# Kernel tuning notes

Hardware: AMD Instinct MI355X
Metric: run time of the kernel (lower is better)

Reference implementation:

```python
import jax, jax.numpy as jnp
import numpy as np
from jax.ops import segment_sum

NEG_SLOPE = 0.01  # torch F.leaky_relu default

N_NODES = 100000
N_EDGES = 1600000
IN_FEAT = 67
HIDDEN = 256
N_CLASS = 18
N_GRAPHS = 256


def setup_inputs() -> dict:
    key = jax.random.key(0)
    ks = jax.random.split(key, 12)
    h = jax.random.normal(ks[0], (N_NODES, IN_FEAT), dtype=jnp.float32)
    src = jax.random.randint(ks[1], (N_EDGES,), 0, N_NODES, dtype=jnp.int32)
    dst = jax.random.randint(ks[2], (N_EDGES,), 0, N_NODES, dtype=jnp.int32)
    graph_ids = jnp.sort(jax.random.randint(ks[3], (N_NODES,), 0, N_GRAPHS, dtype=jnp.int32))
    s = 0.05
    W1_self = jax.random.normal(ks[4], (IN_FEAT, HIDDEN), dtype=jnp.float32) * s
    W1_neigh = jax.random.normal(ks[5], (IN_FEAT, HIDDEN), dtype=jnp.float32) * s
    b1 = jnp.zeros((HIDDEN,), dtype=jnp.float32)
    W2_self = jax.random.normal(ks[6], (HIDDEN, HIDDEN), dtype=jnp.float32) * s
    W2_neigh = jax.random.normal(ks[7], (HIDDEN, HIDDEN), dtype=jnp.float32) * s
    b2 = jnp.zeros((HIDDEN,), dtype=jnp.float32)
    Wfc = jax.random.normal(ks[8], (HIDDEN, N_CLASS), dtype=jnp.float32) * s
    bfc = jnp.zeros((N_CLASS,), dtype=jnp.float32)
    return {
        "h": h, "W1_self": W1_self, "W1_neigh": W1_neigh, "b1": b1,
        "W2_self": W2_self, "W2_neigh": W2_neigh, "b2": b2,
        "Wfc": Wfc, "bfc": bfc,
        "src": src, "dst": dst, "graph_ids": graph_ids, "num_graphs": N_GRAPHS,
    }


def _sage_mean(h, Wself, Wneigh, b, src, dst, n_nodes):
    # DGL SAGEConv(mean): h_neigh = mean over incoming neighbors; 0 if no neighbors
    agg = segment_sum(h[src], dst, num_segments=n_nodes)          # [N, D]
    deg = segment_sum(jnp.ones_like(dst, dtype=h.dtype), dst, num_segments=n_nodes)
    h_neigh = agg / jnp.maximum(deg, 1.0)[:, None]
    return h @ Wself + h_neigh @ Wneigh + b


def reference(h, W1_self, W1_neigh, b1, W2_self, W2_neigh, b2, Wfc, bfc,
              src, dst, graph_ids, num_graphs):
    n_nodes = h.shape[0]
    x = jax.nn.leaky_relu(_sage_mean(h, W1_self, W1_neigh, b1, src, dst, n_nodes), NEG_SLOPE)
    x = jax.nn.leaky_relu(_sage_mean(x, W2_self, W2_neigh, b2, src, dst, n_nodes), NEG_SLOPE)
    # dgl.mean_nodes: per-graph mean pooling over nodes
    gsum = segment_sum(x, graph_ids, num_segments=num_graphs)       # [G, D]
    gcnt = segment_sum(jnp.ones((n_nodes,), dtype=x.dtype), graph_ids, num_segments=num_graphs)
    hg = gsum / jnp.maximum(gcnt, 1.0)[:, None]
    return hg @ Wfc + bfc  # [G, n_classifier]
```

## Files before the change

kernel.cpp:

```cpp
#include <hip/hip_runtime.h>

#define WAVE 64
#define OW 256
#define LDA1 96
#define NCHUNK 64
#define PBITS 15
#define PBINS (1 << PBITS)
#define NPART 4

typedef short bf16x8 __attribute__((ext_vector_type(8)));
typedef float f32x4  __attribute__((ext_vector_type(4)));

__device__ __forceinline__ unsigned short f2bf(float f) {
    unsigned int u = __float_as_uint(f);
    u = (u + 0x7FFF + ((u >> 16) & 1)) >> 16;
    return (unsigned short)u;
}
__device__ __forceinline__ float bf2f(unsigned short u) {
    return __uint_as_float(((unsigned int)u) << 16);
}
__device__ __forceinline__ float bflo(unsigned int u) { return __uint_as_float(u << 16); }
__device__ __forceinline__ float bfhi(unsigned int u) { return __uint_as_float(u & 0xFFFF0000u); }
__device__ __forceinline__ unsigned int packbf(float lo, float hi) {
    return (unsigned int)f2bf(lo) | ((unsigned int)f2bf(hi) << 16);
}
__device__ __forceinline__ float lrelu(float x) { return x > 0.0f ? x : 0.01f * x; }


__device__ __forceinline__ void pack_b_body(const float* __restrict__ Ws,
                                            const float* __restrict__ Wn,
                                            unsigned short* __restrict__ Bb,
                                            int KHALF, int KT_HALF, int idx) {
    int e  = idx & 7;
    int l  = (idx >> 3) & 63;
    int nt = (idx >> 9) & 15;
    int kt = idx >> 13;
    int n  = nt * 16 + (l & 15);
    int kh = (kt < KT_HALF ? kt : kt - KT_HALF) * 32 + (l >> 4) * 8 + e;
    const float* W = (kt < KT_HALF) ? Ws : Wn;
    float v = (kh < KHALF) ? W[(size_t)kh * OW + n] : 0.0f;
    Bb[idx] = f2bf(v);
}

__global__ void prep_kernel(const float* __restrict__ h, unsigned int* __restrict__ hb,
                            int N, int K,
                            const float* __restrict__ W1s, const float* __restrict__ W1n,
                            unsigned short* __restrict__ Bb1,
                            const float* __restrict__ W2s, const float* __restrict__ W2n,
                            unsigned short* __restrict__ Bb2) {
    const int tid = blockIdx.x * blockDim.x + threadIdx.x;
    const int nth = gridDim.x * blockDim.x;

    const int tot_h = N * (LDA1 / 2);
    for (int i = tid; i < tot_h; i += nth) {
        int row = i / (LDA1 / 2);
        int c   = (i - row * (LDA1 / 2)) * 2;
        float v0 = (c     < K) ? h[(size_t)row * K + c]     : 0.0f;
        float v1 = (c + 1 < K) ? h[(size_t)row * K + c + 1] : 0.0f;
        hb[i] = packbf(v0, v1);
    }
    for (int i = tid; i < 2 * 3 * 16 * 64 * 8; i += nth)
        pack_b_body(W1s, W1n, Bb1, K, 3, i);
    for (int i = tid; i < 2 * 8 * 16 * 64 * 8; i += nth)
        pack_b_body(W2s, W2n, Bb2, OW, 8, i);
}


__global__ __launch_bounds__(512) void hist_kernel(const int* __restrict__ dst, int E, int N,
                                                   int* __restrict__ hist,
                                                   unsigned short* __restrict__ rank_local) {
    __shared__ unsigned int lcnt[PBINS / 2];
    const int c    = blockIdx.x / NPART;
    const int p    = blockIdx.x - c * NPART;
    const int base = p << PBITS;
    const int nb   = (N - base < PBINS) ? (N - base) : PBINS;
    if (nb <= 0) return;
    const int che = (E + NCHUNK - 1) / NCHUNK;
    const int beg = c * che;
    const int end = (beg + che < E) ? (beg + che) : E;

    for (int i = threadIdx.x; i < PBINS / 2; i += 512) lcnt[i] = 0;
    __syncthreads();

    for (int e = beg + (int)threadIdx.x; e < end; e += 512) {
        int d = dst[e] - base;
        if ((unsigned)d < (unsigned)nb) {
            unsigned int sh  = (d & 1) * 16;
            unsigned int old = atomicAdd(&lcnt[d >> 1], 1u << sh);
            rank_local[e] = (unsigned short)((old >> sh) & 0xFFFFu);
        }
    }
    __syncthreads();

    int* hrow = hist + (size_t)c * N + base;
    for (int i = threadIdx.x; i < nb; i += 512) {
        unsigned int v = lcnt[i >> 1];
        hrow[i] = (int)((v >> ((i & 1) * 16)) & 0xFFFFu);
    }
}

__global__ void chunk_scan_kernel(int* __restrict__ hist, int* __restrict__ cnt, int N) {
    int bin = blockIdx.x * blockDim.x + threadIdx.x;
    if (bin >= N) return;
    int s = 0;
#pragma unroll 8
    for (int c = 0; c < NCHUNK; ++c) {
        size_t idx = (size_t)c * N + bin;
        int t = hist[idx];
        hist[idx] = s;
        s += t;
    }
    cnt[bin] = s;
}

__global__ __launch_bounds__(1024) void scan_blocksum(const int* __restrict__ cnt,
                                                      int* __restrict__ bsum, int n) {
    __shared__ int s[1024];
    int i = blockIdx.x * 1024 + threadIdx.x;
    s[threadIdx.x] = (i < n) ? cnt[i] : 0;
    __syncthreads();
    for (int off = 512; off > 0; off >>= 1) {
        if (threadIdx.x < off) s[threadIdx.x] += s[threadIdx.x + off];
        __syncthreads();
    }
    if (threadIdx.x == 0) bsum[blockIdx.x] = s[0];
}

__global__ __launch_bounds__(128) void scan_offsets(int* __restrict__ bsum, int nb) {
    __shared__ int s[128];
    int v = (threadIdx.x < nb) ? bsum[threadIdx.x] : 0;
    s[threadIdx.x] = v;
    __syncthreads();
    for (int off = 1; off < 128; off <<= 1) {
        int t = (threadIdx.x >= off) ? s[threadIdx.x - off] : 0;
        __syncthreads();
        s[threadIdx.x] += t;
        __syncthreads();
    }
    if (threadIdx.x < nb) bsum[threadIdx.x] = s[threadIdx.x] - v;
}

__global__ __launch_bounds__(1024) void scan_write(const int* __restrict__ cnt,
                                                   const int* __restrict__ boff,
                                                   int* __restrict__ rowptr, int n) {
    __shared__ int s[1024];
    int i = blockIdx.x * 1024 + threadIdx.x;
    int v = (i < n) ? cnt[i] : 0;
    s[threadIdx.x] = v;
    __syncthreads();
    for (int off = 1; off < 1024; off <<= 1) {
        int t = (threadIdx.x >= off) ? s[threadIdx.x - off] : 0;
        __syncthreads();
        s[threadIdx.x] += t;
        __syncthreads();
    }
    if (i < n) rowptr[i + 1] = boff[blockIdx.x] + s[threadIdx.x];
    if (i == 0) rowptr[0] = 0;
}

__global__ void fill_kernel(const int* __restrict__ src, const int* __restrict__ dst,
                            const unsigned short* __restrict__ rank_local,
                            const int* __restrict__ rowptr, const int* __restrict__ hist,
                            int* __restrict__ csr, int E, int N) {
    const int che = (E + NCHUNK - 1) / NCHUNK;
    const int tid = blockIdx.x * blockDim.x + threadIdx.x;
    const int nth = gridDim.x * blockDim.x;
    for (int e = tid; e < E; e += nth) {
        int d = dst[e];
        int c = e / che;
        int pos = rowptr[d] + hist[(size_t)c * N + d] + (int)rank_local[e];
        csr[pos] = src[e];
    }
}


__global__ void gather_mean256_half(const unsigned int* __restrict__ feat,
                                    const int* __restrict__ rowptr, const int* __restrict__ csr,
                                    unsigned int* __restrict__ aggm, int N, int colhalf) {
    const int lane = threadIdx.x & (WAVE - 1);
    const int grp  = lane >> 4;
    const int sub  = lane & 15;
    const int cb   = colhalf * 64;
    int wave = (blockIdx.x * blockDim.x + threadIdx.x) / WAVE;
    int nw   = (gridDim.x * blockDim.x) / WAVE;

    for (int v = wave; v < N; v += nw) {
        const int beg = rowptr[v], deg = rowptr[v + 1] - beg;
        float l0 = 0.f, h0 = 0.f, l1 = 0.f, h1 = 0.f,
              l2 = 0.f, h2 = 0.f, l3 = 0.f, h3 = 0.f;

        const int noct = deg >> 3;
        for (int i = 0; i < noct; ++i) {
            int e0 = csr[beg + 8 * i + grp];
            int e1 = csr[beg + 8 * i + 4 + grp];
            uint4 x0 = *(const uint4*)(feat + (size_t)e0 * 128 + cb + sub * 4);
            uint4 x1 = *(const uint4*)(feat + (size_t)e1 * 128 + cb + sub * 4);
            l0 += bflo(x0.x) + bflo(x1.x); h0 += bfhi(x0.x) + bfhi(x1.x);
            l1 += bflo(x0.y) + bflo(x1.y); h1 += bfhi(x0.y) + bfhi(x1.y);
            l2 += bflo(x0.z) + bflo(x1.z); h2 += bfhi(x0.z) + bfhi(x1.z);
            l3 += bflo(x0.w) + bflo(x1.w); h3 += bfhi(x0.w) + bfhi(x1.w);
        }
        for (int e = (noct << 3) + grp; e < deg; e += 4) {
            int s = csr[beg + e];
            uint4 x = *(const uint4*)(feat + (size_t)s * 128 + cb + sub * 4);
            l0 += bflo(x.x); h0 += bfhi(x.x);
            l1 += bflo(x.y); h1 += bfhi(x.y);
            l2 += bflo(x.z); h2 += bfhi(x.z);
            l3 += bflo(x.w); h3 += bfhi(x.w);
        }
        l0 += __shfl_xor(l0, 16); l0 += __shfl_xor(l0, 32);
        h0 += __shfl_xor(h0, 16); h0 += __shfl_xor(h0, 32);
        l1 += __shfl_xor(l1, 16); l1 += __shfl_xor(l1, 32);
        h1 += __shfl_xor(h1, 16); h1 += __shfl_xor(h1, 32);
        l2 += __shfl_xor(l2, 16); l2 += __shfl_xor(l2, 32);
        h2 += __shfl_xor(h2, 16); h2 += __shfl_xor(h2, 32);
        l3 += __shfl_xor(l3, 16); l3 += __shfl_xor(l3, 32);
        h3 += __shfl_xor(h3, 16); h3 += __shfl_xor(h3, 32);

        if (grp == 0) {
            float inv = 1.0f / fmaxf((float)deg, 1.0f);
            uint4 o;
            o.x = packbf(l0 * inv, h0 * inv);
            o.y = packbf(l1 * inv, h1 * inv);
            o.z = packbf(l2 * inv, h2 * inv);
            o.w = packbf(l3 * inv, h3 * inv);
            *(uint4*)(aggm + (size_t)v * 128 + cb + sub * 4) = o;
        }
    }
}

__global__ void gather_mean_pad(const unsigned int* __restrict__ feat,
                                const int* __restrict__ rowptr, const int* __restrict__ csr,
                                unsigned int* __restrict__ aggm, int N) {
    const int lane = threadIdx.x & (WAVE - 1);
    const int half = lane >> 5;
    const int sub  = lane & 31;
    const bool act = sub < 24;
    int wave = (blockIdx.x * blockDim.x + threadIdx.x) / WAVE;
    int nw   = (gridDim.x * blockDim.x) / WAVE;

    for (int v = wave; v < N; v += nw) {
        const int beg = rowptr[v], deg = rowptr[v + 1] - beg;
        const int npairs = deg >> 1;
        float l0 = 0.f, h0 = 0.f, l1 = 0.f, h1 = 0.f;

        int p = 0;
        for (; p + 3 < npairs; p += 4) {
            int i0 = csr[beg + 2 * (p + 0) + half];
            int i1 = csr[beg + 2 * (p + 1) + half];
            int i2 = csr[beg + 2 * (p + 2) + half];
            int i3 = csr[beg + 2 * (p + 3) + half];
            if (act) {
                uint2 x0 = *(const uint2*)(feat + (size_t)i0 * 48 + sub * 2);
                uint2 x1 = *(const uint2*)(feat + (size_t)i1 * 48 + sub * 2);
                uint2 x2 = *(const uint2*)(feat + (size_t)i2 * 48 + sub * 2);
                uint2 x3 = *(const uint2*)(feat + (size_t)i3 * 48 + sub * 2);
                l0 += bflo(x0.x) + bflo(x1.x) + bflo(x2.x) + bflo(x3.x);
                h0 += bfhi(x0.x) + bfhi(x1.x) + bfhi(x2.x) + bfhi(x3.x);
                l1 += bflo(x0.y) + bflo(x1.y) + bflo(x2.y) + bflo(x3.y);
                h1 += bfhi(x0.y) + bfhi(x1.y) + bfhi(x2.y) + bfhi(x3.y);
            }
        }
        for (; p < npairs; ++p) {
            int i0 = csr[beg + 2 * p + half];
            if (act) {
                uint2 x0 = *(const uint2*)(feat + (size_t)i0 * 48 + sub * 2);
                l0 += bflo(x0.x); h0 += bfhi(x0.x);
                l1 += bflo(x0.y); h1 += bfhi(x0.y);
            }
        }
        if ((deg & 1) && half == 0) {
            int i0 = csr[beg + deg - 1];
            if (act) {
                uint2 x0 = *(const uint2*)(feat + (size_t)i0 * 48 + sub * 2);
                l0 += bflo(x0.x); h0 += bfhi(x0.x);
                l1 += bflo(x0.y); h1 += bfhi(x0.y);
            }
        }
        l0 += __shfl_xor(l0, 32); h0 += __shfl_xor(h0, 32);
        l1 += __shfl_xor(l1, 32); h1 += __shfl_xor(h1, 32);

        if (half == 0 && act) {
            float inv = 1.0f / fmaxf((float)deg, 1.0f);
            uint2 o;
            o.x = packbf(l0 * inv, h0 * inv);
            o.y = packbf(l1 * inv, h1 * inv);
            *(uint2*)(aggm + (size_t)v * 48 + sub * 2) = o;
        }
    }
}

template<int KT_HALF, int CHUNK>
__global__ __launch_bounds__(256) void sage_mfma(
    const unsigned short* __restrict__ Hs, const unsigned short* __restrict__ Hn, int lda,
    const unsigned short* __restrict__ Bb, const float* __restrict__ bias,
    unsigned short* __restrict__ outb, int M)
{
    constexpr int NT    = 2 * KT_HALF;
    constexpr int NCH   = NT / CHUNK;
    constexpr int CELEM = CHUNK * 16 * 64;
    constexpr int CPT   = CELEM / 256;
    __shared__ bf16x8 Bs[CELEM];

    const int t    = threadIdx.x;
    const int lane = t & 63, wid = t >> 6;
    const int wm   = wid >> 1, wn = wid & 1;
    const int brow = blockIdx.x * 64;
    const int lrow = lane & 15, kblk = lane >> 4;

    const int r0 = brow + wm * 32 + lrow;
    const int r1 = r0 + 16;
    const int r0c = (r0 < M) ? r0 : (M - 1);
    const int r1c = (r1 < M) ? r1 : (M - 1);

    f32x4 acc[2][8];
#pragma unroll
    for (int rt = 0; rt < 2; ++rt)
#pragma unroll
        for (int ct = 0; ct < 8; ++ct) acc[rt][ct] = (f32x4)0.0f;

    for (int ch = 0; ch < NCH; ++ch) {
        bf16x8 a0[CHUNK], a1[CHUNK];
#pragma unroll
        for (int k = 0; k < CHUNK; ++k) {
            int kt = ch * CHUNK + k;
            bool self = kt < KT_HALF;
            int kh = (self ? kt : kt - KT_HALF) * 32 + kblk * 8;
            const unsigned short* srcp = self ? Hs : Hn;
            a0[k] = *(const bf16x8*)(srcp + (size_t)r0c * lda + kh);
            a1[k] = *(const bf16x8*)(srcp + (size_t)r1c * lda + kh);
        }
        const bf16x8* gB = (const bf16x8*)Bb + (size_t)ch * CELEM;
        bf16x8 tmp[CPT];
#pragma unroll
        for (int i = 0; i < CPT; ++i) tmp[i] = gB[i * 256 + t];
        __syncthreads();
#pragma unroll
        for (int i = 0; i < CPT; ++i) Bs[i * 256 + t] = tmp[i];
        __syncthreads();
#pragma unroll
        for (int k = 0; k < CHUNK; ++k) {
            const bf16x8* bp = &Bs[(k * 16 + wn * 8) * 64 + lane];
#pragma unroll
            for (int ct = 0; ct < 8; ++ct) {
                bf16x8 b = bp[ct * 64];
                acc[0][ct] = __builtin_amdgcn_mfma_f32_16x16x32_bf16(a0[k], b, acc[0][ct], 0, 0, 0);
                acc[1][ct] = __builtin_amdgcn_mfma_f32_16x16x32_bf16(a1[k], b, acc[1][ct], 0, 0, 0);
            }
        }
    }

#pragma unroll
    for (int rt = 0; rt < 2; ++rt) {
        int rbase = brow + wm * 32 + rt * 16 + kblk * 4;
#pragma unroll
        for (int ct = 0; ct < 8; ++ct) {
            int col = wn * 128 + ct * 16 + lrow;
            float vb = bias[col];
#pragma unroll
            for (int j = 0; j < 4; ++j) {
                int row = rbase + j;
                if (row < M)
                    outb[(size_t)row * OW + col] = f2bf(lrelu(acc[rt][ct][j] + vb));
            }
        }
    }
}


__global__ __launch_bounds__(256) void pool_fc_kernel(
    const unsigned short* __restrict__ x, const int* __restrict__ gid,
    const float* __restrict__ Wfc, const float* __restrict__ bfc,
    float* __restrict__ out, int N, int C)
{
    int g = blockIdx.x;
    int lo = 0, hi = N;
    while (lo < hi) { int m = (lo + hi) >> 1; if (gid[m] < g) lo = m + 1; else hi = m; }
    int beg = lo;
    hi = N;
    while (lo < hi) { int m = (lo + hi) >> 1; if (gid[m] <= g) lo = m + 1; else hi = m; }
    int end = lo;

    __shared__ float hg[OW];
    int c = threadIdx.x;
    float s0 = 0.f, s1 = 0.f, s2 = 0.f, s3 = 0.f;
    int r = beg;
    for (; r + 3 < end; r += 4) {
        s0 += bf2f(x[(size_t)(r + 0) * OW + c]);
        s1 += bf2f(x[(size_t)(r + 1) * OW + c]);
        s2 += bf2f(x[(size_t)(r + 2) * OW + c]);
        s3 += bf2f(x[(size_t)(r + 3) * OW + c]);
    }
    for (; r < end; ++r) s0 += bf2f(x[(size_t)r * OW + c]);
    float s = (s0 + s1) + (s2 + s3);
    float inv = (end > beg) ? 1.0f / (float)(end - beg) : 0.0f;
    hg[c] = s * inv;
    __syncthreads();

    if (c < C) {
        float a = bfc[c];
        for (int k = 0; k < OW; ++k)
            a = fmaf(hg[k], Wfc[(size_t)k * C + c], a);
        out[(size_t)g * C + c] = a;
    }
}

extern "C" void kernel_launch(void* const* d_in, const int* in_sizes, int n_in,
                              void* d_out, int out_size, void* d_ws, size_t ws_size,
                              hipStream_t stream) {
    const float* h   = (const float*)d_in[0];
    const float* W1s = (const float*)d_in[1];
    const float* W1n = (const float*)d_in[2];
    const float* b1  = (const float*)d_in[3];
    const float* W2s = (const float*)d_in[4];
    const float* W2n = (const float*)d_in[5];
    const float* b2  = (const float*)d_in[6];
    const float* Wfc = (const float*)d_in[7];
    const float* bfc = (const float*)d_in[8];
    const int*   src = (const int*)d_in[9];
    const int*   dst = (const int*)d_in[10];
    const int*   gid = (const int*)d_in[11];

    const int N  = in_sizes[11];
    const int E  = in_sizes[9];
    const int K1 = in_sizes[0] / N;
    const int NC = in_sizes[8];
    const int G  = out_size / NC;

    char* w = (char*)d_ws;
    auto alloc = [&](size_t bytes) { char* p = w; w += (bytes + 255) & ~(size_t)255; return p; };
    unsigned int*   hb     = (unsigned int*)alloc((size_t)N * (LDA1 / 2) * 4);
    unsigned int*   agg1b  = (unsigned int*)alloc((size_t)N * (LDA1 / 2) * 4);
    unsigned short* x1b    = (unsigned short*)alloc((size_t)N * OW * 2);
    unsigned short* agg2b  = (unsigned short*)alloc((size_t)N * OW * 2);
    int*            rowptr = (int*)alloc((size_t)(N + 1) * 4);
    int*            cnt    = (int*)alloc((size_t)N * 4);
    int*            csr    = (int*)alloc((size_t)E * 4);
    unsigned short* rankl  = (unsigned short*)alloc((size_t)E * 2);
    int*            hist   = (int*)alloc((size_t)NCHUNK * N * 4);
    int*            bsum   = (int*)alloc(1024 * 4);
    unsigned short* Bb1    = (unsigned short*)alloc((size_t)2 * 3 * 16 * 64 * 8 * 2);
    unsigned short* Bb2    = (unsigned short*)alloc((size_t)2 * 8 * 16 * 64 * 8 * 2);

    float* out = (float*)d_out;
    const int nb = (N + 1023) / 1024;

    hist_kernel<<<NCHUNK * NPART, 512, 0, stream>>>(dst, E, N, hist, rankl);
    chunk_scan_kernel<<<(N + 255) / 256, 256, 0, stream>>>(hist, cnt, N);
    scan_blocksum<<<nb, 1024, 0, stream>>>(cnt, bsum, N);
    scan_offsets<<<1, 128, 0, stream>>>(bsum, nb);
    scan_write<<<nb, 1024, 0, stream>>>(cnt, bsum, rowptr, N);
    fill_kernel<<<2048, 256, 0, stream>>>(src, dst, rankl, rowptr, hist, csr, E, N);

    prep_kernel<<<2048, 256, 0, stream>>>(h, hb, N, K1, W1s, W1n, Bb1, W2s, W2n, Bb2);

    const int gemm_grid = (N + 63) / 64;

    gather_mean_pad<<<4096, 256, 0, stream>>>(hb, rowptr, csr, agg1b, N);
    sage_mfma<3, 2><<<gemm_grid, 256, 0, stream>>>((const unsigned short*)hb,
                                                   (const unsigned short*)agg1b, LDA1,
                                                   Bb1, b1, x1b, N);

    gather_mean256_half<<<4096, 256, 0, stream>>>((const unsigned int*)x1b, rowptr, csr,
                                                  (unsigned int*)agg2b, N, 0);
    gather_mean256_half<<<4096, 256, 0, stream>>>((const unsigned int*)x1b, rowptr, csr,
                                                  (unsigned int*)agg2b, N, 1);
    sage_mfma<8, 2><<<gemm_grid, 256, 0, stream>>>(x1b, agg2b, OW, Bb2, b2, x1b, N);

    pool_fc_kernel<<<G, 256, 0, stream>>>(x1b, gid, Wfc, bfc, out, N, NC);
}
```

Baseline: 424.5 us.

## Double-buffer weight tiles in SAGE GEMM and shrink edge histogram to 16-bit

The SAGE MFMA GEMM now handles 32 rows per block instead of 64. It double-buffers each 32-wide K-slice of packed weights in LDS and prefetches the next A fragment and B slice while the current MFMAs run, so global loads overlap compute. Separately, the per-chunk destination histogram is stored as 16-bit values instead of 32-bit, which halves its traffic in the hist, scan and fill kernels. The cost is that each output row now re-reads the weight matrix from L2 twice as often, and per-chunk prefix counts must fit in 16 bits.

```diff
diff --git a/kernel.cpp b/kernel.cpp
--- a/kernel.cpp
+++ b/kernel.cpp
@@ -67,7 +67,7 @@
 
 
 __global__ __launch_bounds__(512) void hist_kernel(const int* __restrict__ dst, int E, int N,
-                                                   int* __restrict__ hist,
+                                                   unsigned short* __restrict__ hist,
                                                    unsigned short* __restrict__ rank_local) {
     __shared__ unsigned int lcnt[PBINS / 2];
     const int c    = blockIdx.x / NPART;
@@ -92,14 +92,15 @@
     }
     __syncthreads();
 
-    int* hrow = hist + (size_t)c * N + base;
+    unsigned short* hrow = hist + (size_t)c * N + base;
     for (int i = threadIdx.x; i < nb; i += 512) {
         unsigned int v = lcnt[i >> 1];
-        hrow[i] = (int)((v >> ((i & 1) * 16)) & 0xFFFFu);
-    }
-}
-
-__global__ void chunk_scan_kernel(int* __restrict__ hist, int* __restrict__ cnt, int N) {
+        hrow[i] = (unsigned short)((v >> ((i & 1) * 16)) & 0xFFFFu);
+    }
+}
+
+__global__ void chunk_scan_kernel(unsigned short* __restrict__ hist, int* __restrict__ cnt,
+                                  int N) {
     int bin = blockIdx.x * blockDim.x + threadIdx.x;
     if (bin >= N) return;
     int s = 0;
@@ -107,7 +108,7 @@
     for (int c = 0; c < NCHUNK; ++c) {
         size_t idx = (size_t)c * N + bin;
         int t = hist[idx];
-        hist[idx] = s;
+        hist[idx] = (unsigned short)s;
         s += t;
     }
     cnt[bin] = s;
@@ -160,7 +161,8 @@
 
 __global__ void fill_kernel(const int* __restrict__ src, const int* __restrict__ dst,
                             const unsigned short* __restrict__ rank_local,
-                            const int* __restrict__ rowptr, const int* __restrict__ hist,
+                            const int* __restrict__ rowptr,
+                            const unsigned short* __restrict__ hist,
                             int* __restrict__ csr, int E, int N) {
     const int che = (E + NCHUNK - 1) / NCHUNK;
     const int tid = blockIdx.x * blockDim.x + threadIdx.x;
@@ -168,7 +170,7 @@
     for (int e = tid; e < E; e += nth) {
         int d = dst[e];
         int c = e / che;
-        int pos = rowptr[d] + hist[(size_t)c * N + d] + (int)rank_local[e];
+        int pos = rowptr[d] + (int)hist[(size_t)c * N + d] + (int)rank_local[e];
         csr[pos] = src[e];
     }
 }
@@ -290,79 +292,77 @@
     }
 }
 
-template<int KT_HALF, int CHUNK>
+template<int KT_HALF>
 __global__ __launch_bounds__(256) void sage_mfma(
     const unsigned short* __restrict__ Hs, const unsigned short* __restrict__ Hn, int lda,
     const unsigned short* __restrict__ Bb, const float* __restrict__ bias,
     unsigned short* __restrict__ outb, int M)
 {
-    constexpr int NT    = 2 * KT_HALF;
-    constexpr int NCH   = NT / CHUNK;
-    constexpr int CELEM = CHUNK * 16 * 64;
-    constexpr int CPT   = CELEM / 256;
-    __shared__ bf16x8 Bs[CELEM];
+    constexpr int NT = 2 * KT_HALF;
+    __shared__ bf16x8 Bs[2][1024];
 
     const int t    = threadIdx.x;
     const int lane = t & 63, wid = t >> 6;
     const int wm   = wid >> 1, wn = wid & 1;
-    const int brow = blockIdx.x * 64;
+    const int brow = blockIdx.x * 32;
     const int lrow = lane & 15, kblk = lane >> 4;
 
-    const int r0 = brow + wm * 32 + lrow;
-    const int r1 = r0 + 16;
-    const int r0c = (r0 < M) ? r0 : (M - 1);
-    const int r1c = (r1 < M) ? r1 : (M - 1);
-
-    f32x4 acc[2][8];
-#pragma unroll
-    for (int rt = 0; rt < 2; ++rt)
-#pragma unroll
-        for (int ct = 0; ct < 8; ++ct) acc[rt][ct] = (f32x4)0.0f;
-
-    for (int ch = 0; ch < NCH; ++ch) {
-        bf16x8 a0[CHUNK], a1[CHUNK];
-#pragma unroll
-        for (int k = 0; k < CHUNK; ++k) {
-            int kt = ch * CHUNK + k;
-            bool self = kt < KT_HALF;
-            int kh = (self ? kt : kt - KT_HALF) * 32 + kblk * 8;
-            const unsigned short* srcp = self ? Hs : Hn;
-            a0[k] = *(const bf16x8*)(srcp + (size_t)r0c * lda + kh);
-            a1[k] = *(const bf16x8*)(srcp + (size_t)r1c * lda + kh);
-        }
-        const bf16x8* gB = (const bf16x8*)Bb + (size_t)ch * CELEM;
-        bf16x8 tmp[CPT];
-#pragma unroll
-        for (int i = 0; i < CPT; ++i) tmp[i] = gB[i * 256 + t];
-        __syncthreads();
-#pragma unroll
-        for (int i = 0; i < CPT; ++i) Bs[i * 256 + t] = tmp[i];
-        __syncthreads();
-#pragma unroll
-        for (int k = 0; k < CHUNK; ++k) {
-            const bf16x8* bp = &Bs[(k * 16 + wn * 8) * 64 + lane];
-#pragma unroll
-            for (int ct = 0; ct < 8; ++ct) {
-                bf16x8 b = bp[ct * 64];
-                acc[0][ct] = __builtin_amdgcn_mfma_f32_16x16x32_bf16(a0[k], b, acc[0][ct], 0, 0, 0);
-                acc[1][ct] = __builtin_amdgcn_mfma_f32_16x16x32_bf16(a1[k], b, acc[1][ct], 0, 0, 0);
-            }
-        }
-    }
-
-#pragma unroll
-    for (int rt = 0; rt < 2; ++rt) {
-        int rbase = brow + wm * 32 + rt * 16 + kblk * 4;
+    const int r  = brow + wm * 16 + lrow;
+    const int rc = (r < M) ? r : (M - 1);
+
+    auto loadA = [&](int kt) -> bf16x8 {
+        bool self = kt < KT_HALF;
+        int kh = (self ? kt : kt - KT_HALF) * 32 + kblk * 8;
+        const unsigned short* srcp = self ? Hs : Hn;
+        return *(const bf16x8*)(srcp + (size_t)rc * lda + kh);
+    };
+
+    f32x4 acc[8];
+#pragma unroll
+    for (int ct = 0; ct < 8; ++ct) acc[ct] = (f32x4)0.0f;
+
+    bf16x8 tmp[4];
+    const bf16x8* gB0 = (const bf16x8*)Bb;
+#pragma unroll
+    for (int i = 0; i < 4; ++i) tmp[i] = gB0[i * 256 + t];
+    bf16x8 aCur = loadA(0);
+#pragma unroll
+    for (int i = 0; i < 4; ++i) Bs[0][i * 256 + t] = tmp[i];
+    __syncthreads();
+
+    for (int ch = 0; ch < NT; ++ch) {
+        const bool more = (ch + 1 < NT);
+        bf16x8 aNxt;
+        if (more) {
+            const bf16x8* gB = (const bf16x8*)Bb + (size_t)(ch + 1) * 1024;
+#pragma unroll
+            for (int i = 0; i < 4; ++i) tmp[i] = gB[i * 256 + t];
+            aNxt = loadA(ch + 1);
+        }
+        const bf16x8* bp = &Bs[ch & 1][(wn * 8) * 64 + lane];
 #pragma unroll
         for (int ct = 0; ct < 8; ++ct) {
-            int col = wn * 128 + ct * 16 + lrow;
-            float vb = bias[col];
-#pragma unroll
-            for (int j = 0; j < 4; ++j) {
-                int row = rbase + j;
-                if (row < M)
-                    outb[(size_t)row * OW + col] = f2bf(lrelu(acc[rt][ct][j] + vb));
-            }
+            bf16x8 b = bp[ct * 64];
+            acc[ct] = __builtin_amdgcn_mfma_f32_16x16x32_bf16(aCur, b, acc[ct], 0, 0, 0);
+        }
+        if (more) {
+#pragma unroll
+            for (int i = 0; i < 4; ++i) Bs[(ch + 1) & 1][i * 256 + t] = tmp[i];
+            __syncthreads();
+            aCur = aNxt;
+        }
+    }
+
+    const int rbase = brow + wm * 16 + kblk * 4;
+#pragma unroll
+    for (int ct = 0; ct < 8; ++ct) {
+        int col = wn * 128 + ct * 16 + lrow;
+        float vb = bias[col];
+#pragma unroll
+        for (int j = 0; j < 4; ++j) {
+            int row = rbase + j;
+            if (row < M)
+                outb[(size_t)row * OW + col] = f2bf(lrelu(acc[ct][j] + vb));
         }
     }
 }
@@ -437,7 +437,7 @@
     int*            cnt    = (int*)alloc((size_t)N * 4);
     int*            csr    = (int*)alloc((size_t)E * 4);
     unsigned short* rankl  = (unsigned short*)alloc((size_t)E * 2);
-    int*            hist   = (int*)alloc((size_t)NCHUNK * N * 4);
+    unsigned short* hist   = (unsigned short*)alloc((size_t)NCHUNK * N * 2);
     int*            bsum   = (int*)alloc(1024 * 4);
     unsigned short* Bb1    = (unsigned short*)alloc((size_t)2 * 3 * 16 * 64 * 8 * 2);
     unsigned short* Bb2    = (unsigned short*)alloc((size_t)2 * 8 * 16 * 64 * 8 * 2);
@@ -454,18 +454,18 @@
 
     prep_kernel<<<2048, 256, 0, stream>>>(h, hb, N, K1, W1s, W1n, Bb1, W2s, W2n, Bb2);
 
-    const int gemm_grid = (N + 63) / 64;
+    const int gemm_grid = (N + 31) / 32;
 
     gather_mean_pad<<<4096, 256, 0, stream>>>(hb, rowptr, csr, agg1b, N);
-    sage_mfma<3, 2><<<gemm_grid, 256, 0, stream>>>((const unsigned short*)hb,
-                                                   (const unsigned short*)agg1b, LDA1,
-                                                   Bb1, b1, x1b, N);
+    sage_mfma<3><<<gemm_grid, 256, 0, stream>>>((const unsigned short*)hb,
+                                                (const unsigned short*)agg1b, LDA1,
+                                                Bb1, b1, x1b, N);
 
     gather_mean256_half<<<4096, 256, 0, stream>>>((const unsigned int*)x1b, rowptr, csr,
                                                   (unsigned int*)agg2b, N, 0);
     gather_mean256_half<<<4096, 256, 0, stream>>>((const unsigned int*)x1b, rowptr, csr,
                                                   (unsigned int*)agg2b, N, 1);
-    sage_mfma<8, 2><<<gemm_grid, 256, 0, stream>>>(x1b, agg2b, OW, Bb2, b2, x1b, N);
+    sage_mfma<8><<<gemm_grid, 256, 0, stream>>>(x1b, agg2b, OW, Bb2, b2, x1b, N);
 
     pool_fc_kernel<<<G, 256, 0, stream>>>(x1b, gid, Wfc, bfc, out, N, NC);
 }
```

Measured after the change: 426.5 us. Within noise of the previous version (+0.5%).
